# Kernel optimization log

Hardware: AMD Instinct MI355X
Metric: run time of the kernel (lower is better)

The kernel has to match this reference:

```python
import jax, jax.numpy as jnp
import numpy as np

B, S, E, H = 4, 2048, 512, 8
DK = E // H  # 64 quantum wires per head


def setup_inputs() -> dict:
    key = jax.random.key(0)
    k1, k2, k3, k4 = jax.random.split(key, 4)
    x = jax.random.normal(k1, (B, S, E), dtype=jnp.float32)
    theta = jax.random.normal(k2, (DK,), dtype=jnp.float32)
    W = jax.random.normal(k3, (E, E), dtype=jnp.float32) * (1.0 / np.sqrt(E))
    b = jax.random.normal(k4, (E,), dtype=jnp.float32) * 0.01
    return {"x": x, "theta": theta, "W": W, "b": b}


def _quantum_project(x, theta):
    # x: [B,S,E] -> heads [B,H,S,DK]. Circuit per wire: RX(x_i) then RX(theta_i),
    # product state => <Z_i> = cos(x_i + theta_i).
    xh = x.reshape(B, S, H, DK).transpose(0, 2, 1, 3)  # [B,H,S,DK]
    return jnp.cos(xh + theta)


def reference(x, theta, W, b):
    q = _quantum_project(x, theta)
    k = _quantum_project(x, theta)
    v = _quantum_project(x, theta)
    scores = jnp.einsum('bhqd,bhkd->bhqk', q, k) / jnp.sqrt(jnp.float32(DK))
    attn = jax.nn.softmax(scores, axis=-1)  # dropout is identity in eval
    out = jnp.einsum('bhqk,bhkd->bhqd', attn, v)  # [B,H,S,DK]
    out = out.transpose(0, 2, 1, 3).reshape(B, S, E)
    return out @ W.T + b
```

## Files before the change

### kernel.cpp

```cpp
#include <hip/hip_runtime.h>
#include <hip/hip_bf16.h>
#include <math.h>

#define B_ 4
#define S_ 2048
#define E_ 512
#define H_ 8
#define DK_ 64

typedef __attribute__((ext_vector_type(8))) short short8;
typedef __attribute__((ext_vector_type(4))) short short4_t;
typedef __attribute__((ext_vector_type(4))) float f32x4;
typedef _Float16 half4 __attribute__((ext_vector_type(4)));

using bf16 = __hip_bfloat16;

__device__ inline short8 ld8(const void* p) {
  return *reinterpret_cast<const short8*>(p);
}

static __device__ inline unsigned short f2bs(float f) {
  __hip_bfloat16 h = __float2bfloat16(f);
  return (unsigned short)__builtin_bit_cast(short, h);
}

static __device__ inline short8 cvt8(float4 a, float4 b) {
  short8 r;
  r[0] = f2bs(a.x); r[1] = f2bs(a.y); r[2] = f2bs(a.z); r[3] = f2bs(a.w);
  r[4] = f2bs(b.x); r[5] = f2bs(b.y); r[6] = f2bs(b.z); r[7] = f2bs(b.w);
  return r;
}

__global__ __launch_bounds__(256) void prep_g_kernel(
    const float* __restrict__ x, const float* __restrict__ theta,
    bf16* __restrict__ g, _Float16* __restrict__ gTh) {
  int bh = blockIdx.y;
  int b = bh >> 3, h = bh & 7;
  int s0 = blockIdx.x * 64;
  __shared__ _Float16 tile[64][68];
  int tid = threadIdx.x;
  const float* xp = x + ((size_t)(b * S_ + s0)) * E_ + h * DK_;
  bf16* gp = g + ((size_t)bh * S_ + s0) * DK_;
#pragma unroll
  for (int it = 0; it < 16; ++it) {
    int idx = it * 256 + tid;
    int sr = idx >> 6, dc = idx & 63;
    float val = __cosf(xp[(size_t)sr * E_ + dc] + theta[dc]);
    gp[sr * DK_ + dc] = __float2bfloat16(val);
    tile[sr][dc] = (_Float16)val;
  }
  __syncthreads();
  _Float16* gTp = gTh + ((size_t)bh * DK_) * S_ + s0;
#pragma unroll
  for (int it = 0; it < 16; ++it) {
    int idx = it * 256 + tid;
    int dr = idx >> 6, sc = idx & 63;
    gTp[(size_t)dr * S_ + sc] = tile[sc][dr];
  }
}

__global__ __launch_bounds__(256) void attn_kernel(
    const bf16* __restrict__ g, const _Float16* __restrict__ gTh,
    bf16* __restrict__ ao) {
  const int tid = threadIdx.x;
  const int wave = tid >> 6, lane = tid & 63;
  const int col = lane & 15, quad = lane >> 4;
  const int bh = blockIdx.y;
  const int q0 = blockIdx.x * 128 + wave * 32;
  const bf16* gp = g + (size_t)bh * S_ * DK_;
  const _Float16* gvp = gTh + (size_t)bh * DK_ * S_;

  __shared__ short kt[64 * 72];
  __shared__ _Float16 vt[64 * 72];

  short8 qa[2][2];
#pragma unroll
  for (int qc = 0; qc < 2; ++qc) {
    const bf16* qp = gp + (size_t)(q0 + qc * 16 + col) * DK_ + quad * 8;
    qa[qc][0] = ld8(qp);
    qa[qc][1] = ld8(qp + 32);
  }

  f32x4 o[2][4];
#pragma unroll
  for (int qc = 0; qc < 2; ++qc)
#pragma unroll
    for (int dc = 0; dc < 4; ++dc) o[qc][dc] = f32x4{0.f, 0.f, 0.f, 0.f};
  float l[2] = {0.f, 0.f};

  const float C1 = 0.18033688011112042f;
  const float C2 = 2.8853900817779268f;

  const int srow = tid >> 3;
  const int soct = (tid & 7) * 8;
  const int sd0 = srow * 72 + soct;
  const int sd1 = (srow + 32) * 72 + soct;
  const bf16* kg0 = gp + tid * 8;
  const bf16* kg1 = gp + (tid + 256) * 8;
  const _Float16* vg0 = gvp + (size_t)srow * S_ + (tid & 7) * 8;
  const _Float16* vg1 = gvp + (size_t)(srow + 32) * S_ + (tid & 7) * 8;

  short8 kr0 = ld8(kg0), kr1 = ld8(kg1), vr0 = ld8(vg0), vr1 = ld8(vg1);

  for (int kk = 0; kk < S_; kk += 64) {
    *reinterpret_cast<short8*>(kt + sd0) = kr0;
    *reinterpret_cast<short8*>(kt + sd1) = kr1;
    *reinterpret_cast<short8*>(vt + sd0) = vr0;
    *reinterpret_cast<short8*>(vt + sd1) = vr1;
    __syncthreads();

    if (kk + 64 < S_) {
      kr0 = ld8(kg0 + (kk + 64) * 64);
      kr1 = ld8(kg1 + (kk + 64) * 64);
      vr0 = ld8(vg0 + kk + 64);
      vr1 = ld8(vg1 + kk + 64);
    }

    short8 kf[4][2];
#pragma unroll
    for (int kc = 0; kc < 4; ++kc) {
      const short* kp = kt + (kc * 16 + col) * 72 + quad * 8;
      kf[kc][0] = *reinterpret_cast<const short8*>(kp);
      kf[kc][1] = *reinterpret_cast<const short8*>(kp + 32);
    }

    f32x4 s[2][4];
#pragma unroll
    for (int qc = 0; qc < 2; ++qc)
#pragma unroll
      for (int kc = 0; kc < 4; ++kc) {
        f32x4 z{0.f, 0.f, 0.f, 0.f};
        z = __builtin_amdgcn_mfma_f32_16x16x32_bf16(kf[kc][0], qa[qc][0], z, 0, 0, 0);
        s[qc][kc] = __builtin_amdgcn_mfma_f32_16x16x32_bf16(kf[kc][1], qa[qc][1], z, 0, 0, 0);
      }

    half4 pf[2][4];
#pragma unroll
    for (int qc = 0; qc < 2; ++qc) {
#pragma unroll
      for (int kc = 0; kc < 4; ++kc) {
        float p0 = __builtin_amdgcn_exp2f(__builtin_fmaf(s[qc][kc][0], C1, C2));
        float p1 = __builtin_amdgcn_exp2f(__builtin_fmaf(s[qc][kc][1], C1, C2));
        float p2 = __builtin_amdgcn_exp2f(__builtin_fmaf(s[qc][kc][2], C1, C2));
        float p3 = __builtin_amdgcn_exp2f(__builtin_fmaf(s[qc][kc][3], C1, C2));
        l[qc] += (p0 + p1) + (p2 + p3);
        half4 pk;
        pk[0] = (_Float16)p0; pk[1] = (_Float16)p1;
        pk[2] = (_Float16)p2; pk[3] = (_Float16)p3;
        pf[qc][kc] = pk;
      }
    }

#pragma unroll
    for (int dc = 0; dc < 4; ++dc) {
      half4 vf[4];
#pragma unroll
      for (int kc = 0; kc < 4; ++kc)
        vf[kc] = *reinterpret_cast<const half4*>(vt + (dc * 16 + col) * 72 + kc * 16 + quad * 4);
#pragma unroll
      for (int qc = 0; qc < 2; ++qc)
#pragma unroll
        for (int kc = 0; kc < 4; ++kc)
          o[qc][dc] = __builtin_amdgcn_mfma_f32_16x16x16f16(vf[kc], pf[qc][kc], o[qc][dc], 0, 0, 0);
    }
    __syncthreads();
  }

  int b = bh >> 3, h = bh & 7;
#pragma unroll
  for (int qc = 0; qc < 2; ++qc) {
    float t = l[qc];
    t += __shfl_xor(t, 16);
    t += __shfl_xor(t, 32);
    float inv = __builtin_amdgcn_rcpf(t);
    int row = q0 + qc * 16 + col;
    bf16* op = ao + ((size_t)b * S_ + row) * E_ + h * DK_;
#pragma unroll
    for (int dc = 0; dc < 4; ++dc) {
      short4_t pk;
      pk.x = f2bs(o[qc][dc][0] * inv);
      pk.y = f2bs(o[qc][dc][1] * inv);
      pk.z = f2bs(o[qc][dc][2] * inv);
      pk.w = f2bs(o[qc][dc][3] * inv);
      *reinterpret_cast<short4_t*>(op + dc * 16 + quad * 4) = pk;
    }
  }
}

__global__ __launch_bounds__(256) void proj_kernel(
    const bf16* __restrict__ ao, const float* __restrict__ W,
    const float* __restrict__ bias, float* __restrict__ out) {
  const int tid = threadIdx.x;
  const int wave = tid >> 6, lane = tid & 63;
  const int col = lane & 15, quad = lane >> 4;
  const int m0 = blockIdx.x * 64;
  const int n0 = blockIdx.y * 64;
  __shared__ short at[64 * 72];
  __shared__ short bt[64 * 72];

  const int srow = tid >> 3;
  const int soct = (tid & 7) * 8;
  const int sd0 = srow * 72 + soct;
  const int sd1 = (srow + 32) * 72 + soct;
  const bf16* ag0 = ao + (size_t)(m0 + srow) * E_ + (tid & 7) * 8;
  const bf16* ag1 = ao + (size_t)(m0 + srow + 32) * E_ + (tid & 7) * 8;
  const float* wg0 = W + (size_t)(n0 + srow) * E_ + (tid & 7) * 8;
  const float* wg1 = W + (size_t)(n0 + srow + 32) * E_ + (tid & 7) * 8;

  short8 ar0 = ld8(ag0), ar1 = ld8(ag1);
  float4 w00 = *reinterpret_cast<const float4*>(wg0);
  float4 w01 = *reinterpret_cast<const float4*>(wg0 + 4);
  float4 w10 = *reinterpret_cast<const float4*>(wg1);
  float4 w11 = *reinterpret_cast<const float4*>(wg1 + 4);

  f32x4 acc[4] = {{0.f,0.f,0.f,0.f},{0.f,0.f,0.f,0.f},{0.f,0.f,0.f,0.f},{0.f,0.f,0.f,0.f}};

  for (int k0 = 0; k0 < E_; k0 += 64) {
    *reinterpret_cast<short8*>(at + sd0) = ar0;
    *reinterpret_cast<short8*>(at + sd1) = ar1;
    *reinterpret_cast<short8*>(bt + sd0) = cvt8(w00, w01);
    *reinterpret_cast<short8*>(bt + sd1) = cvt8(w10, w11);
    __syncthreads();
    if (k0 + 64 < E_) {
      ar0 = ld8(ag0 + k0 + 64);
      ar1 = ld8(ag1 + k0 + 64);
      w00 = *reinterpret_cast<const float4*>(wg0 + k0 + 64);
      w01 = *reinterpret_cast<const float4*>(wg0 + k0 + 68);
      w10 = *reinterpret_cast<const float4*>(wg1 + k0 + 64);
      w11 = *reinterpret_cast<const float4*>(wg1 + k0 + 68);
    }
    const short* ap = at + (wave * 16 + col) * 72 + quad * 8;
    short8 a0 = *reinterpret_cast<const short8*>(ap);
    short8 a1 = *reinterpret_cast<const short8*>(ap + 32);
#pragma unroll
    for (int f = 0; f < 4; ++f) {
      const short* bp = bt + (f * 16 + col) * 72 + quad * 8;
      short8 b0 = *reinterpret_cast<const short8*>(bp);
      short8 b1 = *reinterpret_cast<const short8*>(bp + 32);
      acc[f] = __builtin_amdgcn_mfma_f32_16x16x32_bf16(a0, b0, acc[f], 0, 0, 0);
      acc[f] = __builtin_amdgcn_mfma_f32_16x16x32_bf16(a1, b1, acc[f], 0, 0, 0);
    }
    __syncthreads();
  }

#pragma unroll
  for (int f = 0; f < 4; ++f) {
    float bv = bias[n0 + f * 16 + col];
#pragma unroll
    for (int r = 0; r < 4; ++r) {
      int row = m0 + wave * 16 + quad * 4 + r;
      out[(size_t)row * E_ + n0 + f * 16 + col] = acc[f][r] + bv;
    }
  }
}

extern "C" void kernel_launch(void* const* d_in, const int* in_sizes, int n_in,
                              void* d_out, int out_size, void* d_ws, size_t ws_size,
                              hipStream_t stream) {
  const float* x = (const float*)d_in[0];
  const float* theta = (const float*)d_in[1];
  const float* W = (const float*)d_in[2];
  const float* bias = (const float*)d_in[3];
  float* out = (float*)d_out;
  char* ws = (char*)d_ws;
  const size_t gsz = (size_t)B_ * H_ * S_ * DK_ * 2;
  bf16* g = (bf16*)ws;
  _Float16* gTh = (_Float16*)(ws + gsz);
  bf16* ao = (bf16*)(ws + 2 * gsz);

  prep_g_kernel<<<dim3(S_ / 64, B_ * H_), 256, 0, stream>>>(x, theta, g, gTh);
  attn_kernel<<<dim3(S_ / 128, B_ * H_), 256, 0, stream>>>(g, gTh, ao);
  proj_kernel<<<dim3((B_ * S_) / 64, E_ / 64), 256, 0, stream>>>(ao, W, bias, out);
}
```

Baseline: 141.3 us.

## Split keys across waves in attention, switch to fp16, widen projection K tile

The attention kernel now gives each wave 16 keys of every 64-key tile against all 64 queries of the block, rather than each wave owning 32 queries. Partial row sums and outputs are reduced across waves through shared memory at the end. All intermediates move from bf16 to fp16, with the 1/sqrt(dk) scale folded into the fp16 query. The projection kernel stages 128-wide K tiles. This cuts redundant LDS K/V fragment reads per wave and doubles the attention grid, at the cost of an extra cross-wave reduction epilogue and less fp16 range headroom.

```diff
diff --git a/kernel.cpp b/kernel.cpp
--- a/kernel.cpp
+++ b/kernel.cpp
@@ -9,44 +9,37 @@
 #define DK_ 64
 
 typedef __attribute__((ext_vector_type(8))) short short8;
-typedef __attribute__((ext_vector_type(4))) short short4_t;
 typedef __attribute__((ext_vector_type(4))) float f32x4;
+typedef _Float16 half8 __attribute__((ext_vector_type(8)));
 typedef _Float16 half4 __attribute__((ext_vector_type(4)));
-
-using bf16 = __hip_bfloat16;
 
 __device__ inline short8 ld8(const void* p) {
   return *reinterpret_cast<const short8*>(p);
 }
 
-static __device__ inline unsigned short f2bs(float f) {
-  __hip_bfloat16 h = __float2bfloat16(f);
-  return (unsigned short)__builtin_bit_cast(short, h);
-}
-
-static __device__ inline short8 cvt8(float4 a, float4 b) {
-  short8 r;
-  r[0] = f2bs(a.x); r[1] = f2bs(a.y); r[2] = f2bs(a.z); r[3] = f2bs(a.w);
-  r[4] = f2bs(b.x); r[5] = f2bs(b.y); r[6] = f2bs(b.z); r[7] = f2bs(b.w);
-  return r;
+static __device__ inline short8 cvt8h(float4 a, float4 b) {
+  half8 r;
+  r[0] = (_Float16)a.x; r[1] = (_Float16)a.y; r[2] = (_Float16)a.z; r[3] = (_Float16)a.w;
+  r[4] = (_Float16)b.x; r[5] = (_Float16)b.y; r[6] = (_Float16)b.z; r[7] = (_Float16)b.w;
+  return __builtin_bit_cast(short8, r);
 }
 
 __global__ __launch_bounds__(256) void prep_g_kernel(
     const float* __restrict__ x, const float* __restrict__ theta,
-    bf16* __restrict__ g, _Float16* __restrict__ gTh) {
+    _Float16* __restrict__ g, _Float16* __restrict__ gTh) {
   int bh = blockIdx.y;
   int b = bh >> 3, h = bh & 7;
   int s0 = blockIdx.x * 64;
   __shared__ _Float16 tile[64][68];
   int tid = threadIdx.x;
   const float* xp = x + ((size_t)(b * S_ + s0)) * E_ + h * DK_;
-  bf16* gp = g + ((size_t)bh * S_ + s0) * DK_;
+  _Float16* gp = g + ((size_t)bh * S_ + s0) * DK_;
 #pragma unroll
   for (int it = 0; it < 16; ++it) {
     int idx = it * 256 + tid;
     int sr = idx >> 6, dc = idx & 63;
     float val = __cosf(xp[(size_t)sr * E_ + dc] + theta[dc]);
-    gp[sr * DK_ + dc] = __float2bfloat16(val);
+    gp[sr * DK_ + dc] = (_Float16)val;
     tile[sr][dc] = (_Float16)val;
   }
   __syncthreads();
@@ -59,48 +52,51 @@
   }
 }
 
-__global__ __launch_bounds__(256) void attn_kernel(
-    const bf16* __restrict__ g, const _Float16* __restrict__ gTh,
-    bf16* __restrict__ ao) {
+__global__ __launch_bounds__(256, 3) void attn_kernel(
+    const _Float16* __restrict__ g, const _Float16* __restrict__ gTh,
+    _Float16* __restrict__ ao) {
   const int tid = threadIdx.x;
   const int wave = tid >> 6, lane = tid & 63;
   const int col = lane & 15, quad = lane >> 4;
   const int bh = blockIdx.y;
-  const int q0 = blockIdx.x * 128 + wave * 32;
-  const bf16* gp = g + (size_t)bh * S_ * DK_;
+  const int q0 = blockIdx.x * 64;
+  const _Float16* gp = g + (size_t)bh * S_ * DK_;
   const _Float16* gvp = gTh + (size_t)bh * DK_ * S_;
 
-  __shared__ short kt[64 * 72];
-  __shared__ _Float16 vt[64 * 72];
-
-  short8 qa[2][2];
-#pragma unroll
-  for (int qc = 0; qc < 2; ++qc) {
-    const bf16* qp = gp + (size_t)(q0 + qc * 16 + col) * DK_ + quad * 8;
-    qa[qc][0] = ld8(qp);
-    qa[qc][1] = ld8(qp + 32);
-  }
-
-  f32x4 o[2][4];
-#pragma unroll
-  for (int qc = 0; qc < 2; ++qc)
-#pragma unroll
-    for (int dc = 0; dc < 4; ++dc) o[qc][dc] = f32x4{0.f, 0.f, 0.f, 0.f};
-  float l[2] = {0.f, 0.f};
-
-  const float C1 = 0.18033688011112042f;
-  const float C2 = 2.8853900817779268f;
+  __shared__ short smem[2 * 64 * 72];
+  short* kt = smem;
+  short* vt = smem + 64 * 72;
 
   const int srow = tid >> 3;
   const int soct = (tid & 7) * 8;
   const int sd0 = srow * 72 + soct;
   const int sd1 = (srow + 32) * 72 + soct;
-  const bf16* kg0 = gp + tid * 8;
-  const bf16* kg1 = gp + (tid + 256) * 8;
+  const _Float16* kg0 = gp + tid * 8;
+  const _Float16* kg1 = gp + (tid + 256) * 8;
   const _Float16* vg0 = gvp + (size_t)srow * S_ + (tid & 7) * 8;
   const _Float16* vg1 = gvp + (size_t)(srow + 32) * S_ + (tid & 7) * 8;
 
   short8 kr0 = ld8(kg0), kr1 = ld8(kg1), vr0 = ld8(vg0), vr1 = ld8(vg1);
+
+  *reinterpret_cast<short8*>(kt + sd0) = ld8(gp + (size_t)q0 * DK_ + tid * 8);
+  *reinterpret_cast<short8*>(kt + sd1) = ld8(gp + (size_t)q0 * DK_ + (tid + 256) * 8);
+  __syncthreads();
+  const _Float16 hC1 = (_Float16)0.18033688011112042f;
+  half8 qa[4][2];
+#pragma unroll
+  for (int qc = 0; qc < 4; ++qc) {
+    const short* qp = kt + (qc * 16 + col) * 72 + quad * 8;
+    qa[qc][0] = *reinterpret_cast<const half8*>(qp) * hC1;
+    qa[qc][1] = *reinterpret_cast<const half8*>(qp + 32) * hC1;
+  }
+  __syncthreads();
+
+  f32x4 o[4][4];
+#pragma unroll
+  for (int qc = 0; qc < 4; ++qc)
+#pragma unroll
+    for (int dc = 0; dc < 4; ++dc) o[qc][dc] = f32x4{0.f, 0.f, 0.f, 0.f};
+  float l[4] = {0.f, 0.f, 0.f, 0.f};
 
   for (int kk = 0; kk < S_; kk += 64) {
     *reinterpret_cast<short8*>(kt + sd0) = kr0;
@@ -116,129 +112,137 @@
       vr1 = ld8(vg1 + kk + 64);
     }
 
-    short8 kf[4][2];
-#pragma unroll
-    for (int kc = 0; kc < 4; ++kc) {
-      const short* kp = kt + (kc * 16 + col) * 72 + quad * 8;
-      kf[kc][0] = *reinterpret_cast<const short8*>(kp);
-      kf[kc][1] = *reinterpret_cast<const short8*>(kp + 32);
-    }
-
-    f32x4 s[2][4];
-#pragma unroll
-    for (int qc = 0; qc < 2; ++qc)
-#pragma unroll
-      for (int kc = 0; kc < 4; ++kc) {
-        f32x4 z{0.f, 0.f, 0.f, 0.f};
-        z = __builtin_amdgcn_mfma_f32_16x16x32_bf16(kf[kc][0], qa[qc][0], z, 0, 0, 0);
-        s[qc][kc] = __builtin_amdgcn_mfma_f32_16x16x32_bf16(kf[kc][1], qa[qc][1], z, 0, 0, 0);
-      }
-
-    half4 pf[2][4];
-#pragma unroll
-    for (int qc = 0; qc < 2; ++qc) {
-#pragma unroll
-      for (int kc = 0; kc < 4; ++kc) {
-        float p0 = __builtin_amdgcn_exp2f(__builtin_fmaf(s[qc][kc][0], C1, C2));
-        float p1 = __builtin_amdgcn_exp2f(__builtin_fmaf(s[qc][kc][1], C1, C2));
-        float p2 = __builtin_amdgcn_exp2f(__builtin_fmaf(s[qc][kc][2], C1, C2));
-        float p3 = __builtin_amdgcn_exp2f(__builtin_fmaf(s[qc][kc][3], C1, C2));
-        l[qc] += (p0 + p1) + (p2 + p3);
-        half4 pk;
-        pk[0] = (_Float16)p0; pk[1] = (_Float16)p1;
-        pk[2] = (_Float16)p2; pk[3] = (_Float16)p3;
-        pf[qc][kc] = pk;
-      }
+    const short* kp = kt + (wave * 16 + col) * 72 + quad * 8;
+    half8 kf0 = *reinterpret_cast<const half8*>(kp);
+    half8 kf1 = *reinterpret_cast<const half8*>(kp + 32);
+
+    half4 pf[4];
+#pragma unroll
+    for (int qc = 0; qc < 4; ++qc) {
+      f32x4 z{0.f, 0.f, 0.f, 0.f};
+      z = __builtin_amdgcn_mfma_f32_16x16x32_f16(kf0, qa[qc][0], z, 0, 0, 0);
+      z = __builtin_amdgcn_mfma_f32_16x16x32_f16(kf1, qa[qc][1], z, 0, 0, 0);
+      float p0 = __builtin_amdgcn_exp2f(z[0]);
+      float p1 = __builtin_amdgcn_exp2f(z[1]);
+      float p2 = __builtin_amdgcn_exp2f(z[2]);
+      float p3 = __builtin_amdgcn_exp2f(z[3]);
+      l[qc] += (p0 + p1) + (p2 + p3);
+      half4 pk;
+      pk[0] = (_Float16)p0; pk[1] = (_Float16)p1;
+      pk[2] = (_Float16)p2; pk[3] = (_Float16)p3;
+      pf[qc] = pk;
     }
 
 #pragma unroll
     for (int dc = 0; dc < 4; ++dc) {
-      half4 vf[4];
-#pragma unroll
-      for (int kc = 0; kc < 4; ++kc)
-        vf[kc] = *reinterpret_cast<const half4*>(vt + (dc * 16 + col) * 72 + kc * 16 + quad * 4);
-#pragma unroll
-      for (int qc = 0; qc < 2; ++qc)
-#pragma unroll
-        for (int kc = 0; kc < 4; ++kc)
-          o[qc][dc] = __builtin_amdgcn_mfma_f32_16x16x16f16(vf[kc], pf[qc][kc], o[qc][dc], 0, 0, 0);
-    }
-    __syncthreads();
-  }
-
-  int b = bh >> 3, h = bh & 7;
-#pragma unroll
-  for (int qc = 0; qc < 2; ++qc) {
+      half4 vf = *reinterpret_cast<const half4*>(
+          vt + (dc * 16 + col) * 72 + wave * 16 + quad * 4);
+#pragma unroll
+      for (int qc = 0; qc < 4; ++qc)
+        o[qc][dc] = __builtin_amdgcn_mfma_f32_16x16x16f16(vf, pf[qc], o[qc][dc], 0, 0, 0);
+    }
+    __syncthreads();
+  }
+
+#pragma unroll
+  for (int qc = 0; qc < 4; ++qc) {
     float t = l[qc];
     t += __shfl_xor(t, 16);
     t += __shfl_xor(t, 32);
-    float inv = __builtin_amdgcn_rcpf(t);
-    int row = q0 + qc * 16 + col;
-    bf16* op = ao + ((size_t)b * S_ + row) * E_ + h * DK_;
-#pragma unroll
-    for (int dc = 0; dc < 4; ++dc) {
-      short4_t pk;
-      pk.x = f2bs(o[qc][dc][0] * inv);
-      pk.y = f2bs(o[qc][dc][1] * inv);
-      pk.z = f2bs(o[qc][dc][2] * inv);
-      pk.w = f2bs(o[qc][dc][3] * inv);
-      *reinterpret_cast<short4_t*>(op + dc * 16 + quad * 4) = pk;
+    l[qc] = t;
+  }
+  float* red = (float*)smem;
+  if (quad == 0) {
+#pragma unroll
+    for (int qc = 0; qc < 4; ++qc) red[(wave * 4 + qc) * 16 + col] = l[qc];
+  }
+  __syncthreads();
+  float ltot = 0.f;
+#pragma unroll
+  for (int w2 = 0; w2 < 4; ++w2) ltot += red[(w2 * 4 + wave) * 16 + col];
+  float inv = __builtin_amdgcn_rcpf(ltot);
+
+  int b = bh >> 3, h = bh & 7;
+  float* ored = (float*)smem;
+#pragma unroll
+  for (int qc = 0; qc < 4; ++qc) {
+    __syncthreads();
+#pragma unroll
+    for (int dc = 0; dc < 4; ++dc)
+      *reinterpret_cast<f32x4*>(ored + wave * 1024 + lane * 16 + dc * 4) = o[qc][dc];
+    __syncthreads();
+    if (wave == qc) {
+      _Float16* op = ao + ((size_t)b * S_ + (q0 + qc * 16 + col)) * E_ + h * DK_;
+#pragma unroll
+      for (int dc = 0; dc < 4; ++dc) {
+        f32x4 acc = *reinterpret_cast<const f32x4*>(ored + lane * 16 + dc * 4);
+#pragma unroll
+        for (int w2 = 1; w2 < 4; ++w2)
+          acc = acc + *reinterpret_cast<const f32x4*>(ored + w2 * 1024 + lane * 16 + dc * 4);
+        half4 pk;
+        pk[0] = (_Float16)(acc[0] * inv);
+        pk[1] = (_Float16)(acc[1] * inv);
+        pk[2] = (_Float16)(acc[2] * inv);
+        pk[3] = (_Float16)(acc[3] * inv);
+        *reinterpret_cast<half4*>(op + dc * 16 + quad * 4) = pk;
+      }
     }
   }
 }
 
 __global__ __launch_bounds__(256) void proj_kernel(
-    const bf16* __restrict__ ao, const float* __restrict__ W,
+    const _Float16* __restrict__ ao, const float* __restrict__ W,
     const float* __restrict__ bias, float* __restrict__ out) {
   const int tid = threadIdx.x;
   const int wave = tid >> 6, lane = tid & 63;
   const int col = lane & 15, quad = lane >> 4;
   const int m0 = blockIdx.x * 64;
   const int n0 = blockIdx.y * 64;
-  __shared__ short at[64 * 72];
-  __shared__ short bt[64 * 72];
-
-  const int srow = tid >> 3;
-  const int soct = (tid & 7) * 8;
-  const int sd0 = srow * 72 + soct;
-  const int sd1 = (srow + 32) * 72 + soct;
-  const bf16* ag0 = ao + (size_t)(m0 + srow) * E_ + (tid & 7) * 8;
-  const bf16* ag1 = ao + (size_t)(m0 + srow + 32) * E_ + (tid & 7) * 8;
-  const float* wg0 = W + (size_t)(n0 + srow) * E_ + (tid & 7) * 8;
-  const float* wg1 = W + (size_t)(n0 + srow + 32) * E_ + (tid & 7) * 8;
-
-  short8 ar0 = ld8(ag0), ar1 = ld8(ag1);
-  float4 w00 = *reinterpret_cast<const float4*>(wg0);
-  float4 w01 = *reinterpret_cast<const float4*>(wg0 + 4);
-  float4 w10 = *reinterpret_cast<const float4*>(wg1);
-  float4 w11 = *reinterpret_cast<const float4*>(wg1 + 4);
+  __shared__ short at[64 * 136];
+  __shared__ short bt[64 * 136];
+
+  const int srw = tid >> 4;
+  const int soff = (tid & 15) * 8;
+
+  short8 ap_[4];
+  float4 wp_[4][2];
+#pragma unroll
+  for (int it = 0; it < 4; ++it) {
+    int row = it * 16 + srw;
+    ap_[it] = ld8(ao + (size_t)(m0 + row) * E_ + soff);
+    wp_[it][0] = *reinterpret_cast<const float4*>(W + (size_t)(n0 + row) * E_ + soff);
+    wp_[it][1] = *reinterpret_cast<const float4*>(W + (size_t)(n0 + row) * E_ + soff + 4);
+  }
 
   f32x4 acc[4] = {{0.f,0.f,0.f,0.f},{0.f,0.f,0.f,0.f},{0.f,0.f,0.f,0.f},{0.f,0.f,0.f,0.f}};
 
-  for (int k0 = 0; k0 < E_; k0 += 64) {
-    *reinterpret_cast<short8*>(at + sd0) = ar0;
-    *reinterpret_cast<short8*>(at + sd1) = ar1;
-    *reinterpret_cast<short8*>(bt + sd0) = cvt8(w00, w01);
-    *reinterpret_cast<short8*>(bt + sd1) = cvt8(w10, w11);
-    __syncthreads();
-    if (k0 + 64 < E_) {
-      ar0 = ld8(ag0 + k0 + 64);
-      ar1 = ld8(ag1 + k0 + 64);
-      w00 = *reinterpret_cast<const float4*>(wg0 + k0 + 64);
-      w01 = *reinterpret_cast<const float4*>(wg0 + k0 + 68);
-      w10 = *reinterpret_cast<const float4*>(wg1 + k0 + 64);
-      w11 = *reinterpret_cast<const float4*>(wg1 + k0 + 68);
-    }
-    const short* ap = at + (wave * 16 + col) * 72 + quad * 8;
-    short8 a0 = *reinterpret_cast<const short8*>(ap);
-    short8 a1 = *reinterpret_cast<const short8*>(ap + 32);
-#pragma unroll
-    for (int f = 0; f < 4; ++f) {
-      const short* bp = bt + (f * 16 + col) * 72 + quad * 8;
-      short8 b0 = *reinterpret_cast<const short8*>(bp);
-      short8 b1 = *reinterpret_cast<const short8*>(bp + 32);
-      acc[f] = __builtin_amdgcn_mfma_f32_16x16x32_bf16(a0, b0, acc[f], 0, 0, 0);
-      acc[f] = __builtin_amdgcn_mfma_f32_16x16x32_bf16(a1, b1, acc[f], 0, 0, 0);
+  for (int k0 = 0; k0 < E_; k0 += 128) {
+#pragma unroll
+    for (int it = 0; it < 4; ++it) {
+      int row = it * 16 + srw;
+      *reinterpret_cast<short8*>(at + row * 136 + soff) = ap_[it];
+      *reinterpret_cast<short8*>(bt + row * 136 + soff) = cvt8h(wp_[it][0], wp_[it][1]);
+    }
+    __syncthreads();
+    if (k0 + 128 < E_) {
+#pragma unroll
+      for (int it = 0; it < 4; ++it) {
+        int row = it * 16 + srw;
+        ap_[it] = ld8(ao + (size_t)(m0 + row) * E_ + k0 + 128 + soff);
+        wp_[it][0] = *reinterpret_cast<const float4*>(W + (size_t)(n0 + row) * E_ + k0 + 128 + soff);
+        wp_[it][1] = *reinterpret_cast<const float4*>(W + (size_t)(n0 + row) * E_ + k0 + 132 + soff);
+      }
+    }
+#pragma unroll
+    for (int ks = 0; ks < 4; ++ks) {
+      const short* ap = at + (wave * 16 + col) * 136 + ks * 32 + quad * 8;
+      half8 a = *reinterpret_cast<const half8*>(ap);
+#pragma unroll
+      for (int f = 0; f < 4; ++f) {
+        const short* bp = bt + (f * 16 + col) * 136 + ks * 32 + quad * 8;
+        half8 bb = *reinterpret_cast<const half8*>(bp);
+        acc[f] = __builtin_amdgcn_mfma_f32_16x16x32_f16(a, bb, acc[f], 0, 0, 0);
+      }
     }
     __syncthreads();
   }
@@ -264,11 +268,11 @@
   float* out = (float*)d_out;
   char* ws = (char*)d_ws;
   const size_t gsz = (size_t)B_ * H_ * S_ * DK_ * 2;
-  bf16* g = (bf16*)ws;
+  _Float16* g = (_Float16*)ws;
   _Float16* gTh = (_Float16*)(ws + gsz);
-  bf16* ao = (bf16*)(ws + 2 * gsz);
+  _Float16* ao = (_Float16*)(ws + 2 * gsz);
 
   prep_g_kernel<<<dim3(S_ / 64, B_ * H_), 256, 0, stream>>>(x, theta, g, gTh);
-  attn_kernel<<<dim3(S_ / 128, B_ * H_), 256, 0, stream>>>(g, gTh, ao);
+  attn_kernel<<<dim3(S_ / 64, B_ * H_), 256, 0, stream>>>(g, gTh, ao);
   proj_kernel<<<dim3((B_ * S_) / 64, E_ / 64), 256, 0, stream>>>(ao, W, bias, out);
 }
```

Result: faster. 137.1 us (-3.0%).
